# Optimization experiments

Measured on AMD Instinct MI355X. Metric: run time of the kernel, lower is better.

The kernel has to match this reference:

```python
import jax, jax.numpy as jnp
import numpy as np

LN_EPS = 1e-5

def _ln(x, g, b):
    m = jnp.mean(x, axis=-1, keepdims=True)
    v = jnp.mean(jnp.square(x - m), axis=-1, keepdims=True)
    return (x - m) / jnp.sqrt(v + LN_EPS) * g + b

def setup_inputs() -> dict:
    key = jax.random.key(0)
    ks = jax.random.split(key, 24)
    B, S, N = 8, 4096, 32
    H = 32          # self_dim // 2
    D = 64          # self_dim
    O = 32          # output_dim
    def w(k, shape):
        fan_in = shape[0]
        return jax.random.normal(k, shape, dtype=jnp.float32) / np.sqrt(fan_in)
    inp = {
        "expr": jax.random.normal(ks[0], (B, S), dtype=jnp.float32),
        "neighbors": jax.random.normal(ks[1], (B, N, S), dtype=jnp.float32),
        "edge_info": jax.random.normal(ks[2], (B, S, N), dtype=jnp.float32),
        "mask": jax.random.bernoulli(ks[3], 0.1, (B, S)),
        # neighbors branch: Linear(2,H), LN(H), ReLU, Linear(H,H)
        "nW1": w(ks[4], (2, H)), "nb1": jnp.zeros((H,), jnp.float32),
        "nlg": jnp.ones((H,), jnp.float32), "nlb": jnp.zeros((H,), jnp.float32),
        "nW2": w(ks[5], (H, H)), "nb2": jnp.zeros((H,), jnp.float32),
        # self branch: Linear(1,H), LN(H), ReLU, Linear(H,H)
        "sW1": w(ks[6], (1, H)), "sb1": jnp.zeros((H,), jnp.float32),
        "slg": jnp.ones((H,), jnp.float32), "slb": jnp.zeros((H,), jnp.float32),
        "sW2": w(ks[7], (H, H)), "sb2": jnp.zeros((H,), jnp.float32),
        # shared: Linear(D,D), LN(D), ReLU, Linear(D,O)
        "hW1": w(ks[8], (D, D)), "hb1": jnp.zeros((D,), jnp.float32),
        "hlg": jnp.ones((D,), jnp.float32), "hlb": jnp.zeros((D,), jnp.float32),
        "hW2": w(ks[9], (D, O)), "hb2": jnp.zeros((O,), jnp.float32),
    }
    return inp

def reference(expr, neighbors, edge_info, mask,
              nW1, nb1, nlg, nlb, nW2, nb2,
              sW1, sb1, slg, slb, sW2, sb2,
              hW1, hb1, hlg, hlb, hW2, hb2):
    # neighbors: (B,N,S) -> (B,S,N); pair with edge_info -> (B,S,N,2)
    nfeat = jnp.stack([jnp.transpose(neighbors, (0, 2, 1)), edge_info], axis=-1)
    h = nfeat @ nW1 + nb1                      # (B,S,N,H)
    h = jax.nn.relu(_ln(h, nlg, nlb))
    h = h @ nW2 + nb2
    nagg = jnp.sum(h, axis=-2)                 # (B,S,H)
    # self branch
    e = expr[..., None]                        # (B,S,1)
    e = e @ sW1 + sb1                          # (B,S,H)
    e = jax.nn.relu(_ln(e, slg, slb))
    e = e @ sW2 + sb2
    # shared
    x = jnp.concatenate([e, nagg], axis=-1)    # (B,S,2H)
    x = x @ hW1 + hb1
    x = jax.nn.relu(_ln(x, hlg, hlb))
    x = x @ hW2 + hb2                          # (B,S,O)
    x = jnp.where(mask[..., None], 0.0, x)
    return x
```

## Files before the change

### kernel.cpp

```cpp
#include <hip/hip_runtime.h>
#include <hip/hip_bf16.h>


#define LN_EPS 1e-5f

__global__ __launch_bounds__(256) void gnn_fold(
    const float* __restrict__ nW1, const float* __restrict__ nb1,
    const float* __restrict__ nlg, const float* __restrict__ nlb,
    const float* __restrict__ nW2, const float* __restrict__ nb2,
    const float* __restrict__ sW1, const float* __restrict__ sb1,
    const float* __restrict__ slg, const float* __restrict__ slb,
    const float* __restrict__ sW2, const float* __restrict__ sb2,
    const float* __restrict__ hW1, const float* __restrict__ hb1,
    float* __restrict__ ws)
{
    int tid = blockIdx.x * 256 + threadIdx.x;
    int k = tid >> 6, m = tid & 63;
    float acc = 0.f;
    if (k < 32) {
        #pragma unroll 8
        for (int i = 0; i < 32; ++i) acc = fmaf(sW2[k*32 + i], hW1[i*64 + m], acc);
    } else {
        int kk = k - 32;
        #pragma unroll 8
        for (int i = 0; i < 32; ++i) acc = fmaf(nW2[kk*32 + i], hW1[(32 + i)*64 + m], acc);
    }
    ws[256 + k*64 + m] = acc;

    if (blockIdx.x == 0) {
        int t = threadIdx.x;
        if (t < 64) {
            float c = hb1[t];
            for (int i = 0; i < 32; ++i) {
                c = fmaf(sb2[i], hW1[i*64 + t], c);
                c = fmaf(32.f * nb2[i], hW1[(32 + i)*64 + t], c);
            }
            ws[4352 + t] = c;
        } else if (t < 96) {
            int j = t - 64;
            float m0 = 0.f, m1 = 0.f, mb = 0.f;
            for (int i = 0; i < 32; ++i) { m0 += nW1[i]; m1 += nW1[32 + i]; mb += nb1[i]; }
            m0 *= (1.f/32.f); m1 *= (1.f/32.f); mb *= (1.f/32.f);
            float a = nW1[j] - m0, c = nW1[32 + j] - m1, d = nb1[j] - mb;
            ws[j]       = a * nlg[j];
            ws[32 + j]  = c * nlg[j];
            ws[64 + j]  = d * nlg[j];
            ws[96 + j]  = nlb[j];
            float ms = 0.f, msb = 0.f;
            for (int i = 0; i < 32; ++i) { ms += sW1[i]; msb += sb1[i]; }
            ms *= (1.f/32.f); msb *= (1.f/32.f);
            float as = sW1[j] - ms, ds = sb1[j] - msb;
            ws[136 + j] = as * slg[j];
            ws[168 + j] = ds * slg[j];
            ws[200 + j] = slb[j];
        } else if (t == 96) {
            float m0 = 0.f, m1 = 0.f, mb = 0.f;
            for (int i = 0; i < 32; ++i) { m0 += nW1[i]; m1 += nW1[32 + i]; mb += nb1[i]; }
            m0 *= (1.f/32.f); m1 *= (1.f/32.f); mb *= (1.f/32.f);
            float qaa=0,qcc=0,qdd=0,qac=0,qad=0,qcd=0;
            for (int j = 0; j < 32; ++j) {
                float a = nW1[j] - m0, c = nW1[32 + j] - m1, d = nb1[j] - mb;
                qaa += a*a; qcc += c*c; qdd += d*d; qac += a*c; qad += a*d; qcd += c*d;
            }
            ws[128]=qaa*(1.f/32.f); ws[129]=qcc*(1.f/32.f); ws[130]=qdd*(1.f/32.f);
            ws[131]=qac*(1.f/32.f); ws[132]=qad*(1.f/32.f); ws[133]=qcd*(1.f/32.f);
            float ms = 0.f, msb = 0.f;
            for (int i = 0; i < 32; ++i) { ms += sW1[i]; msb += sb1[i]; }
            ms *= (1.f/32.f); msb *= (1.f/32.f);
            float saa=0, sad=0, sdd=0;
            for (int j = 0; j < 32; ++j) {
                float as = sW1[j] - ms, ds = sb1[j] - msb;
                saa += as*as; sad += as*ds; sdd += ds*ds;
            }
            ws[232]=saa*(1.f/32.f); ws[233]=sad*(1.f/32.f); ws[234]=sdd*(1.f/32.f);
        }
    }
}

__global__ __launch_bounds__(256) void gnn_main(
    const float* __restrict__ expr, const float* __restrict__ neighbors,
    const float* __restrict__ edge_info, const int* __restrict__ mask,
    const float* __restrict__ hlg, const float* __restrict__ hlb,
    const float* __restrict__ hW2, const float* __restrict__ hb2,
    const float* __restrict__ ws, float* __restrict__ out)
{
    __shared__ float s_feat[64 * 33 * 2];
    __shared__ float s_inv[64 * 33];
    __shared__ float s_X[64 * 65];
    __shared__ float s_red[64 * 9];
    __shared__ float s_expr[64];
    __shared__ float s_prm[256];
    __shared__ float s_G[64 * 64];
    __shared__ float s_cv[64];
    __shared__ float s_h2[64 * 32];
    __shared__ float s_hb2[32];
    __shared__ float s_hlg[64];
    __shared__ float s_hlb[64];

    const int t  = threadIdx.x;
    const int g0 = blockIdx.x * 64;
    const int bb = g0 >> 12;
    const int s0 = g0 & 4095;
    const float* nbp = neighbors + ((size_t)bb * 32 * 4096 + s0);
    const float* eip = edge_info + (size_t)g0 * 32;

    if (t < 64) ((float4*)s_prm)[t] = ((const float4*)ws)[t];
    #pragma unroll
    for (int i = 0; i < 4; ++i)
        ((float4*)s_G)[i * 256 + t] = ((const float4*)(ws + 256))[i * 256 + t];
    if (t < 16) ((float4*)s_cv)[t] = ((const float4*)(ws + 4352))[t];
    #pragma unroll
    for (int i = 0; i < 2; ++i)
        ((float4*)s_h2)[i * 256 + t] = ((const float4*)hW2)[i * 256 + t];
    if (t < 32) s_hb2[t] = hb2[t];
    if (t < 64) { s_hlg[t] = hlg[t]; s_hlb[t] = hlb[t]; }

    #pragma unroll
    for (int i = 0; i < 8; ++i) {
        int idx = i * 256 + t;
        int n = idx >> 6, col = idx & 63;
        s_feat[(col * 33 + n) * 2 + 0] = nbp[n * 4096 + col];
    }
    #pragma unroll
    for (int i = 0; i < 8; ++i) {
        int idx = i * 256 + t;
        int tok = idx >> 5, n = idx & 31;
        s_feat[(tok * 33 + n) * 2 + 1] = eip[idx];
    }
    if (t < 64) s_expr[t] = expr[g0 + t];
    __syncthreads();

    {
        float qaa = s_prm[128], qcc = s_prm[129], qdd = s_prm[130];
        float qac = s_prm[131], qad = s_prm[132], qcd = s_prm[133];
        #pragma unroll
        for (int i = 0; i < 8; ++i) {
            int idx = i * 256 + t;
            int tok = idx >> 5, n = idx & 31;
            float2 f = *(const float2*)&s_feat[(tok * 33 + n) * 2];
            float nb = f.x, ei = f.y;
            float v = qdd + nb * (qaa * nb + 2.f * qad) + ei * (qcc * ei + 2.f * qcd)
                    + 2.f * qac * nb * ei;
            s_inv[tok * 33 + n] = rsqrtf(v + LN_EPS);
        }
    }
    __syncthreads();

    const int tok = t >> 2;
    const int jb  = (t & 3) * 8;
    float Ag[8], Cg[8], Dg[8], lbv[8];
    *(float4*)&Ag[0]  = *(const float4*)&s_prm[jb];
    *(float4*)&Ag[4]  = *(const float4*)&s_prm[jb + 4];
    *(float4*)&Cg[0]  = *(const float4*)&s_prm[32 + jb];
    *(float4*)&Cg[4]  = *(const float4*)&s_prm[32 + jb + 4];
    *(float4*)&Dg[0]  = *(const float4*)&s_prm[64 + jb];
    *(float4*)&Dg[4]  = *(const float4*)&s_prm[64 + jb + 4];
    *(float4*)&lbv[0] = *(const float4*)&s_prm[96 + jb];
    *(float4*)&lbv[4] = *(const float4*)&s_prm[96 + jb + 4];

    float nsum[8] = {0,0,0,0,0,0,0,0};
    #pragma unroll 4
    for (int n = 0; n < 32; ++n) {
        float2 f  = *(const float2*)&s_feat[(tok * 33 + n) * 2];
        float inv = s_inv[tok * 33 + n];
        #pragma unroll
        for (int i = 0; i < 8; ++i) {
            float r = fmaf(f.x, Ag[i], Dg[i]);
            r = fmaf(f.y, Cg[i], r);
            r = fmaf(r, inv, lbv[i]);
            nsum[i] += fmaxf(r, 0.f);
        }
    }

    {
        float As[8], Ds[8], Lb[8];
        *(float4*)&As[0] = *(const float4*)&s_prm[136 + jb];
        *(float4*)&As[4] = *(const float4*)&s_prm[136 + jb + 4];
        *(float4*)&Ds[0] = *(const float4*)&s_prm[168 + jb];
        *(float4*)&Ds[4] = *(const float4*)&s_prm[168 + jb + 4];
        *(float4*)&Lb[0] = *(const float4*)&s_prm[200 + jb];
        *(float4*)&Lb[4] = *(const float4*)&s_prm[200 + jb + 4];
        float ex  = s_expr[tok];
        float saa = s_prm[232], sad = s_prm[233], sdd = s_prm[234];
        float vs  = fmaf(ex, fmaf(ex, saa, 2.f * sad), sdd);
        float invs = rsqrtf(vs + LN_EPS);
        #pragma unroll
        for (int i = 0; i < 8; ++i) {
            float r = fmaf(ex, As[i], Ds[i]);
            r = fmaf(r, invs, Lb[i]);
            s_X[tok * 65 + jb + i]      = fmaxf(r, 0.f);
            s_X[tok * 65 + 32 + jb + i] = nsum[i];
        }
    }
    __syncthreads();

    const int w = __builtin_amdgcn_readfirstlane(t >> 6);
    const int l = t & 63;
    float y[16];
    *(float4*)&y[0]  = *(const float4*)&s_cv[w * 16];
    *(float4*)&y[4]  = *(const float4*)&s_cv[w * 16 + 4];
    *(float4*)&y[8]  = *(const float4*)&s_cv[w * 16 + 8];
    *(float4*)&y[12] = *(const float4*)&s_cv[w * 16 + 12];
    #pragma unroll 4
    for (int k = 0; k < 64; ++k) {
        float xk = s_X[l * 65 + k];
        const float* gk = &s_G[k * 64 + w * 16];
        float4 g0 = *(const float4*)&gk[0];
        float4 g1 = *(const float4*)&gk[4];
        float4 g2 = *(const float4*)&gk[8];
        float4 g3 = *(const float4*)&gk[12];
        y[0]  = fmaf(xk, g0.x, y[0]);  y[1]  = fmaf(xk, g0.y, y[1]);
        y[2]  = fmaf(xk, g0.z, y[2]);  y[3]  = fmaf(xk, g0.w, y[3]);
        y[4]  = fmaf(xk, g1.x, y[4]);  y[5]  = fmaf(xk, g1.y, y[5]);
        y[6]  = fmaf(xk, g1.z, y[6]);  y[7]  = fmaf(xk, g1.w, y[7]);
        y[8]  = fmaf(xk, g2.x, y[8]);  y[9]  = fmaf(xk, g2.y, y[9]);
        y[10] = fmaf(xk, g2.z, y[10]); y[11] = fmaf(xk, g2.w, y[11]);
        y[12] = fmaf(xk, g3.x, y[12]); y[13] = fmaf(xk, g3.y, y[13]);
        y[14] = fmaf(xk, g3.z, y[14]); y[15] = fmaf(xk, g3.w, y[15]);
    }

    float sm = 0.f, s2 = 0.f;
    #pragma unroll
    for (int i = 0; i < 16; ++i) { sm += y[i]; s2 = fmaf(y[i], y[i], s2); }
    s_red[l * 9 + w * 2 + 0] = sm;
    s_red[l * 9 + w * 2 + 1] = s2;
    __syncthreads();
    float tot = 0.f, tot2 = 0.f;
    #pragma unroll
    for (int r = 0; r < 4; ++r) {
        tot  += s_red[l * 9 + r * 2 + 0];
        tot2 += s_red[l * 9 + r * 2 + 1];
    }
    float mean = tot * (1.f / 64.f);
    float var  = tot2 * (1.f / 64.f) - mean * mean;
    float linv = rsqrtf(var + LN_EPS);
    #pragma unroll
    for (int i = 0; i < 16; ++i) {
        float v = (y[i] - mean) * linv;
        v = fmaf(v, s_hlg[w * 16 + i], s_hlb[w * 16 + i]);
        y[i] = fmaxf(v, 0.f);
    }
    #pragma unroll
    for (int i = 0; i < 16; ++i) s_X[l * 65 + w * 16 + i] = y[i];
    __syncthreads();

    const int ob = w * 8;
    float o[8];
    *(float4*)&o[0] = *(const float4*)&s_hb2[ob];
    *(float4*)&o[4] = *(const float4*)&s_hb2[ob + 4];
    #pragma unroll 4
    for (int m = 0; m < 64; ++m) {
        float ym = s_X[l * 65 + m];
        const float* h2 = &s_h2[m * 32 + ob];
        float4 h0 = *(const float4*)&h2[0];
        float4 h1 = *(const float4*)&h2[4];
        o[0] = fmaf(ym, h0.x, o[0]); o[1] = fmaf(ym, h0.y, o[1]);
        o[2] = fmaf(ym, h0.z, o[2]); o[3] = fmaf(ym, h0.w, o[3]);
        o[4] = fmaf(ym, h1.x, o[4]); o[5] = fmaf(ym, h1.y, o[5]);
        o[6] = fmaf(ym, h1.z, o[6]); o[7] = fmaf(ym, h1.w, o[7]);
    }
    int mk = mask[g0 + l];
    float4 o0 = make_float4(o[0], o[1], o[2], o[3]);
    float4 o1 = make_float4(o[4], o[5], o[6], o[7]);
    if (mk) { o0 = make_float4(0.f,0.f,0.f,0.f); o1 = o0; }
    float4* op = (float4*)(out + (size_t)(g0 + l) * 32 + ob);
    op[0] = o0;
    op[1] = o1;
}

extern "C" void kernel_launch(void* const* d_in, const int* in_sizes, int n_in,
                              void* d_out, int out_size, void* d_ws, size_t ws_size,
                              hipStream_t stream) {
    const float* expr      = (const float*)d_in[0];
    const float* neighbors = (const float*)d_in[1];
    const float* edge_info = (const float*)d_in[2];
    const int*   mask      = (const int*)d_in[3];
    const float* nW1 = (const float*)d_in[4];
    const float* nb1 = (const float*)d_in[5];
    const float* nlg = (const float*)d_in[6];
    const float* nlb = (const float*)d_in[7];
    const float* nW2 = (const float*)d_in[8];
    const float* nb2 = (const float*)d_in[9];
    const float* sW1 = (const float*)d_in[10];
    const float* sb1 = (const float*)d_in[11];
    const float* slg = (const float*)d_in[12];
    const float* slb = (const float*)d_in[13];
    const float* sW2 = (const float*)d_in[14];
    const float* sb2 = (const float*)d_in[15];
    const float* hW1 = (const float*)d_in[16];
    const float* hb1 = (const float*)d_in[17];
    const float* hlg = (const float*)d_in[18];
    const float* hlb = (const float*)d_in[19];
    const float* hW2 = (const float*)d_in[20];
    const float* hb2 = (const float*)d_in[21];
    float* ws  = (float*)d_ws;
    float* out = (float*)d_out;

    gnn_fold<<<16, 256, 0, stream>>>(nW1, nb1, nlg, nlb, nW2, nb2,
                                     sW1, sb1, slg, slb, sW2, sb2,
                                     hW1, hb1, ws);
    gnn_main<<<512, 256, 0, stream>>>(expr, neighbors, edge_info, mask,
                                      hlg, hlb, hW2, hb2, ws, out);
}
```

Baseline: 123.6 us.

## Fuse weight-folding prologue into main kernel and retile the shared-layer GEMM

Removes the separate fold kernel and has every block recompute the folded parameters (LN coefficients via wave shuffles, the 64x64 folded weight matrix, the bias vector) in shared memory, saving one launch and a global workspace round trip. The per-neighbor LN inverse-std is now computed inline in the aggregation loop, which drops a shared buffer and a barrier. The hW1 stage is retiled so each thread handles two tokens by eight outputs. The cost is redundant per-block weight folding (512 blocks each do a 64x64x32 product) plus heavier shared-memory use.

```diff
diff --git a/kernel.cpp b/kernel.cpp
--- a/kernel.cpp
+++ b/kernel.cpp
@@ -1,10 +1,11 @@
 #include <hip/hip_runtime.h>
-#include <hip/hip_bf16.h>
 
 
 #define LN_EPS 1e-5f
 
-__global__ __launch_bounds__(256) void gnn_fold(
+__global__ __launch_bounds__(256) void gnn_fused(
+    const float* __restrict__ expr, const float* __restrict__ neighbors,
+    const float* __restrict__ edge_info, const int* __restrict__ mask,
     const float* __restrict__ nW1, const float* __restrict__ nb1,
     const float* __restrict__ nlg, const float* __restrict__ nlb,
     const float* __restrict__ nW2, const float* __restrict__ nb2,
@@ -12,90 +13,17 @@
     const float* __restrict__ slg, const float* __restrict__ slb,
     const float* __restrict__ sW2, const float* __restrict__ sb2,
     const float* __restrict__ hW1, const float* __restrict__ hb1,
-    float* __restrict__ ws)
-{
-    int tid = blockIdx.x * 256 + threadIdx.x;
-    int k = tid >> 6, m = tid & 63;
-    float acc = 0.f;
-    if (k < 32) {
-        #pragma unroll 8
-        for (int i = 0; i < 32; ++i) acc = fmaf(sW2[k*32 + i], hW1[i*64 + m], acc);
-    } else {
-        int kk = k - 32;
-        #pragma unroll 8
-        for (int i = 0; i < 32; ++i) acc = fmaf(nW2[kk*32 + i], hW1[(32 + i)*64 + m], acc);
-    }
-    ws[256 + k*64 + m] = acc;
-
-    if (blockIdx.x == 0) {
-        int t = threadIdx.x;
-        if (t < 64) {
-            float c = hb1[t];
-            for (int i = 0; i < 32; ++i) {
-                c = fmaf(sb2[i], hW1[i*64 + t], c);
-                c = fmaf(32.f * nb2[i], hW1[(32 + i)*64 + t], c);
-            }
-            ws[4352 + t] = c;
-        } else if (t < 96) {
-            int j = t - 64;
-            float m0 = 0.f, m1 = 0.f, mb = 0.f;
-            for (int i = 0; i < 32; ++i) { m0 += nW1[i]; m1 += nW1[32 + i]; mb += nb1[i]; }
-            m0 *= (1.f/32.f); m1 *= (1.f/32.f); mb *= (1.f/32.f);
-            float a = nW1[j] - m0, c = nW1[32 + j] - m1, d = nb1[j] - mb;
-            ws[j]       = a * nlg[j];
-            ws[32 + j]  = c * nlg[j];
-            ws[64 + j]  = d * nlg[j];
-            ws[96 + j]  = nlb[j];
-            float ms = 0.f, msb = 0.f;
-            for (int i = 0; i < 32; ++i) { ms += sW1[i]; msb += sb1[i]; }
-            ms *= (1.f/32.f); msb *= (1.f/32.f);
-            float as = sW1[j] - ms, ds = sb1[j] - msb;
-            ws[136 + j] = as * slg[j];
-            ws[168 + j] = ds * slg[j];
-            ws[200 + j] = slb[j];
-        } else if (t == 96) {
-            float m0 = 0.f, m1 = 0.f, mb = 0.f;
-            for (int i = 0; i < 32; ++i) { m0 += nW1[i]; m1 += nW1[32 + i]; mb += nb1[i]; }
-            m0 *= (1.f/32.f); m1 *= (1.f/32.f); mb *= (1.f/32.f);
-            float qaa=0,qcc=0,qdd=0,qac=0,qad=0,qcd=0;
-            for (int j = 0; j < 32; ++j) {
-                float a = nW1[j] - m0, c = nW1[32 + j] - m1, d = nb1[j] - mb;
-                qaa += a*a; qcc += c*c; qdd += d*d; qac += a*c; qad += a*d; qcd += c*d;
-            }
-            ws[128]=qaa*(1.f/32.f); ws[129]=qcc*(1.f/32.f); ws[130]=qdd*(1.f/32.f);
-            ws[131]=qac*(1.f/32.f); ws[132]=qad*(1.f/32.f); ws[133]=qcd*(1.f/32.f);
-            float ms = 0.f, msb = 0.f;
-            for (int i = 0; i < 32; ++i) { ms += sW1[i]; msb += sb1[i]; }
-            ms *= (1.f/32.f); msb *= (1.f/32.f);
-            float saa=0, sad=0, sdd=0;
-            for (int j = 0; j < 32; ++j) {
-                float as = sW1[j] - ms, ds = sb1[j] - msb;
-                saa += as*as; sad += as*ds; sdd += ds*ds;
-            }
-            ws[232]=saa*(1.f/32.f); ws[233]=sad*(1.f/32.f); ws[234]=sdd*(1.f/32.f);
-        }
-    }
-}
-
-__global__ __launch_bounds__(256) void gnn_main(
-    const float* __restrict__ expr, const float* __restrict__ neighbors,
-    const float* __restrict__ edge_info, const int* __restrict__ mask,
     const float* __restrict__ hlg, const float* __restrict__ hlb,
     const float* __restrict__ hW2, const float* __restrict__ hb2,
-    const float* __restrict__ ws, float* __restrict__ out)
+    float* __restrict__ out)
 {
     __shared__ float s_feat[64 * 33 * 2];
-    __shared__ float s_inv[64 * 33];
     __shared__ float s_X[64 * 65];
-    __shared__ float s_red[64 * 9];
+    __shared__ float s_G[64 * 64];
+    __shared__ float s_h2[64 * 32];
+    __shared__ float s_tmp[2 * 32 * 36];
+    __shared__ float s_prm[512];
     __shared__ float s_expr[64];
-    __shared__ float s_prm[256];
-    __shared__ float s_G[64 * 64];
-    __shared__ float s_cv[64];
-    __shared__ float s_h2[64 * 32];
-    __shared__ float s_hb2[32];
-    __shared__ float s_hlg[64];
-    __shared__ float s_hlb[64];
 
     const int t  = threadIdx.x;
     const int g0 = blockIdx.x * 64;
@@ -104,17 +32,6 @@
     const float* nbp = neighbors + ((size_t)bb * 32 * 4096 + s0);
     const float* eip = edge_info + (size_t)g0 * 32;
 
-    if (t < 64) ((float4*)s_prm)[t] = ((const float4*)ws)[t];
-    #pragma unroll
-    for (int i = 0; i < 4; ++i)
-        ((float4*)s_G)[i * 256 + t] = ((const float4*)(ws + 256))[i * 256 + t];
-    if (t < 16) ((float4*)s_cv)[t] = ((const float4*)(ws + 4352))[t];
-    #pragma unroll
-    for (int i = 0; i < 2; ++i)
-        ((float4*)s_h2)[i * 256 + t] = ((const float4*)hW2)[i * 256 + t];
-    if (t < 32) s_hb2[t] = hb2[t];
-    if (t < 64) { s_hlg[t] = hlg[t]; s_hlb[t] = hlb[t]; }
-
     #pragma unroll
     for (int i = 0; i < 8; ++i) {
         int idx = i * 256 + t;
@@ -128,51 +45,134 @@
         s_feat[(tok * 33 + n) * 2 + 1] = eip[idx];
     }
     if (t < 64) s_expr[t] = expr[g0 + t];
+    #pragma unroll
+    for (int i = 0; i < 2; ++i)
+        ((float4*)s_h2)[i * 256 + t] = ((const float4*)hW2)[i * 256 + t];
+    if (t < 64) { s_prm[256 + t] = hlg[t]; s_prm[320 + t] = hlb[t]; }
+    if (t < 32) s_prm[384 + t] = hb2[t];
+    #pragma unroll
+    for (int rep = 0; rep < 4; ++rep) {
+        int idx = rep * 256 + t;
+        int i2 = idx & 31, k2 = idx >> 5;
+        s_tmp[i2 * 36 + k2]        = sW2[idx];
+        s_tmp[1152 + i2 * 36 + k2] = nW2[idx];
+    }
+
+    if (t < 32) {
+        const int j = t;
+        float w0 = nW1[j], w1 = nW1[32 + j], b1v = nb1[j];
+        float sw = sW1[j], sb = sb1[j];
+        float m0 = w0, m1 = w1, mb = b1v, ms = sw, msb = sb;
+        #pragma unroll
+        for (int off = 1; off < 32; off <<= 1) {
+            m0  += __shfl_xor(m0, off);
+            m1  += __shfl_xor(m1, off);
+            mb  += __shfl_xor(mb, off);
+            ms  += __shfl_xor(ms, off);
+            msb += __shfl_xor(msb, off);
+        }
+        m0 *= (1.f/32.f); m1 *= (1.f/32.f); mb *= (1.f/32.f);
+        ms *= (1.f/32.f); msb *= (1.f/32.f);
+        float a = w0 - m0, c = w1 - m1, d = b1v - mb;
+        float gj = nlg[j];
+        s_prm[j]      = a * gj;
+        s_prm[32 + j] = c * gj;
+        s_prm[64 + j] = d * gj;
+        s_prm[96 + j] = nlb[j];
+        float as = sw - ms, ds = sb - msb;
+        float sgj = slg[j];
+        s_prm[136 + j] = as * sgj;
+        s_prm[168 + j] = ds * sgj;
+        s_prm[200 + j] = slb[j];
+        float qaa=a*a, qcc=c*c, qdd=d*d, qac=a*c, qad=a*d, qcd=c*d;
+        float saa=as*as, sad=as*ds, sdd=ds*ds;
+        #pragma unroll
+        for (int off = 1; off < 32; off <<= 1) {
+            qaa += __shfl_xor(qaa, off); qcc += __shfl_xor(qcc, off);
+            qdd += __shfl_xor(qdd, off); qac += __shfl_xor(qac, off);
+            qad += __shfl_xor(qad, off); qcd += __shfl_xor(qcd, off);
+            saa += __shfl_xor(saa, off); sad += __shfl_xor(sad, off);
+            sdd += __shfl_xor(sdd, off);
+        }
+        if (j == 0) {
+            s_prm[128]=qaa*(1.f/32.f); s_prm[129]=qcc*(1.f/32.f); s_prm[130]=qdd*(1.f/32.f);
+            s_prm[131]=qac*(1.f/32.f); s_prm[132]=qad*(1.f/32.f); s_prm[133]=qcd*(1.f/32.f);
+            s_prm[232]=saa*(1.f/32.f); s_prm[233]=sad*(1.f/32.f); s_prm[234]=sdd*(1.f/32.f);
+        }
+    }
     __syncthreads();
 
     {
-        float qaa = s_prm[128], qcc = s_prm[129], qdd = s_prm[130];
-        float qac = s_prm[131], qad = s_prm[132], qcd = s_prm[133];
-        #pragma unroll
-        for (int i = 0; i < 8; ++i) {
-            int idx = i * 256 + t;
-            int tok = idx >> 5, n = idx & 31;
+        const int w = t >> 6;
+        const int m = t & 63;
+        const float* hcol = hW1 + m + ((w < 2) ? 0 : 32 * 64);
+        const float* wbase = (w < 2) ? (s_tmp + w * 16) : (s_tmp + 1152 + (w - 2) * 16);
+        float g[16];
+        #pragma unroll
+        for (int kk = 0; kk < 16; ++kk) g[kk] = 0.f;
+        #pragma unroll 4
+        for (int i = 0; i < 32; ++i) {
+            float hv = hcol[i * 64];
+            const float* wr = wbase + i * 36;
+            float4 wa = *(const float4*)&wr[0];
+            float4 wb = *(const float4*)&wr[4];
+            float4 wc = *(const float4*)&wr[8];
+            float4 wd = *(const float4*)&wr[12];
+            g[0]=fmaf(wa.x,hv,g[0]);  g[1]=fmaf(wa.y,hv,g[1]);
+            g[2]=fmaf(wa.z,hv,g[2]);  g[3]=fmaf(wa.w,hv,g[3]);
+            g[4]=fmaf(wb.x,hv,g[4]);  g[5]=fmaf(wb.y,hv,g[5]);
+            g[6]=fmaf(wb.z,hv,g[6]);  g[7]=fmaf(wb.w,hv,g[7]);
+            g[8]=fmaf(wc.x,hv,g[8]);  g[9]=fmaf(wc.y,hv,g[9]);
+            g[10]=fmaf(wc.z,hv,g[10]); g[11]=fmaf(wc.w,hv,g[11]);
+            g[12]=fmaf(wd.x,hv,g[12]); g[13]=fmaf(wd.y,hv,g[13]);
+            g[14]=fmaf(wd.z,hv,g[14]); g[15]=fmaf(wd.w,hv,g[15]);
+        }
+        const int k0 = w * 16;
+        #pragma unroll
+        for (int kk = 0; kk < 16; ++kk) s_G[(k0 + kk) * 64 + m] = g[kk];
+    }
+    if (t >= 192) {
+        const int m = t - 192;
+        float c = hb1[m];
+        #pragma unroll 4
+        for (int i = 0; i < 32; ++i) {
+            c = fmaf(sb2[i], hW1[i * 64 + m], c);
+            c = fmaf(32.f * nb2[i], hW1[(32 + i) * 64 + m], c);
+        }
+        s_prm[416 + m] = c;
+    }
+
+    {
+        const int tok = t >> 2;
+        const int jb  = (t & 3) * 8;
+        float Ag[8], Cg[8], Dg[8], lbv[8];
+        *(float4*)&Ag[0]  = *(const float4*)&s_prm[jb];
+        *(float4*)&Ag[4]  = *(const float4*)&s_prm[jb + 4];
+        *(float4*)&Cg[0]  = *(const float4*)&s_prm[32 + jb];
+        *(float4*)&Cg[4]  = *(const float4*)&s_prm[32 + jb + 4];
+        *(float4*)&Dg[0]  = *(const float4*)&s_prm[64 + jb];
+        *(float4*)&Dg[4]  = *(const float4*)&s_prm[64 + jb + 4];
+        *(float4*)&lbv[0] = *(const float4*)&s_prm[96 + jb];
+        *(float4*)&lbv[4] = *(const float4*)&s_prm[96 + jb + 4];
+        const float qaa = s_prm[128], qcc = s_prm[129], qdd = s_prm[130];
+        const float qac = s_prm[131], qad = s_prm[132], qcd = s_prm[133];
+
+        float nsum[8] = {0,0,0,0,0,0,0,0};
+        #pragma unroll 4
+        for (int n = 0; n < 32; ++n) {
             float2 f = *(const float2*)&s_feat[(tok * 33 + n) * 2];
-            float nb = f.x, ei = f.y;
-            float v = qdd + nb * (qaa * nb + 2.f * qad) + ei * (qcc * ei + 2.f * qcd)
-                    + 2.f * qac * nb * ei;
-            s_inv[tok * 33 + n] = rsqrtf(v + LN_EPS);
-        }
-    }
-    __syncthreads();
-
-    const int tok = t >> 2;
-    const int jb  = (t & 3) * 8;
-    float Ag[8], Cg[8], Dg[8], lbv[8];
-    *(float4*)&Ag[0]  = *(const float4*)&s_prm[jb];
-    *(float4*)&Ag[4]  = *(const float4*)&s_prm[jb + 4];
-    *(float4*)&Cg[0]  = *(const float4*)&s_prm[32 + jb];
-    *(float4*)&Cg[4]  = *(const float4*)&s_prm[32 + jb + 4];
-    *(float4*)&Dg[0]  = *(const float4*)&s_prm[64 + jb];
-    *(float4*)&Dg[4]  = *(const float4*)&s_prm[64 + jb + 4];
-    *(float4*)&lbv[0] = *(const float4*)&s_prm[96 + jb];
-    *(float4*)&lbv[4] = *(const float4*)&s_prm[96 + jb + 4];
-
-    float nsum[8] = {0,0,0,0,0,0,0,0};
-    #pragma unroll 4
-    for (int n = 0; n < 32; ++n) {
-        float2 f  = *(const float2*)&s_feat[(tok * 33 + n) * 2];
-        float inv = s_inv[tok * 33 + n];
-        #pragma unroll
-        for (int i = 0; i < 8; ++i) {
-            float r = fmaf(f.x, Ag[i], Dg[i]);
-            r = fmaf(f.y, Cg[i], r);
-            r = fmaf(r, inv, lbv[i]);
-            nsum[i] += fmaxf(r, 0.f);
-        }
-    }
-
-    {
+            float v = qdd + f.x * fmaf(qaa, f.x, 2.f * qad)
+                    + f.y * fmaf(qcc, f.y, 2.f * qcd)
+                    + 2.f * qac * f.x * f.y;
+            float inv = rsqrtf(v + LN_EPS);
+            #pragma unroll
+            for (int i = 0; i < 8; ++i) {
+                float r = fmaf(f.x, Ag[i], Dg[i]);
+                r = fmaf(f.y, Cg[i], r);
+                r = fmaf(r, inv, lbv[i]);
+                nsum[i] += fmaxf(r, 0.f);
+            }
+        }
         float As[8], Ds[8], Lb[8];
         *(float4*)&As[0] = *(const float4*)&s_prm[136 + jb];
         *(float4*)&As[4] = *(const float4*)&s_prm[136 + jb + 4];
@@ -180,9 +180,8 @@
         *(float4*)&Ds[4] = *(const float4*)&s_prm[168 + jb + 4];
         *(float4*)&Lb[0] = *(const float4*)&s_prm[200 + jb];
         *(float4*)&Lb[4] = *(const float4*)&s_prm[200 + jb + 4];
-        float ex  = s_expr[tok];
-        float saa = s_prm[232], sad = s_prm[233], sdd = s_prm[234];
-        float vs  = fmaf(ex, fmaf(ex, saa, 2.f * sad), sdd);
+        float ex = s_expr[tok];
+        float vs = fmaf(ex, fmaf(ex, s_prm[232], 2.f * s_prm[233]), s_prm[234]);
         float invs = rsqrtf(vs + LN_EPS);
         #pragma unroll
         for (int i = 0; i < 8; ++i) {
@@ -194,83 +193,113 @@
     }
     __syncthreads();
 
-    const int w = __builtin_amdgcn_readfirstlane(t >> 6);
-    const int l = t & 63;
-    float y[16];
-    *(float4*)&y[0]  = *(const float4*)&s_cv[w * 16];
-    *(float4*)&y[4]  = *(const float4*)&s_cv[w * 16 + 4];
-    *(float4*)&y[8]  = *(const float4*)&s_cv[w * 16 + 8];
-    *(float4*)&y[12] = *(const float4*)&s_cv[w * 16 + 12];
+    const int w4 = __builtin_amdgcn_readfirstlane(t >> 6);
+    const int l  = t & 63;
+    const int gi = w4 * 2 + (l >> 5);
+    const int tl = (l & 31) * 2;
+    float y0[8], y1[8];
+    {
+        float4 c0 = *(const float4*)&s_prm[416 + 8 * gi];
+        float4 c1 = *(const float4*)&s_prm[416 + 8 * gi + 4];
+        y0[0]=c0.x; y0[1]=c0.y; y0[2]=c0.z; y0[3]=c0.w;
+        y0[4]=c1.x; y0[5]=c1.y; y0[6]=c1.z; y0[7]=c1.w;
+        #pragma unroll
+        for (int i = 0; i < 8; ++i) y1[i] = y0[i];
+    }
     #pragma unroll 4
     for (int k = 0; k < 64; ++k) {
-        float xk = s_X[l * 65 + k];
-        const float* gk = &s_G[k * 64 + w * 16];
-        float4 g0 = *(const float4*)&gk[0];
-        float4 g1 = *(const float4*)&gk[4];
-        float4 g2 = *(const float4*)&gk[8];
-        float4 g3 = *(const float4*)&gk[12];
-        y[0]  = fmaf(xk, g0.x, y[0]);  y[1]  = fmaf(xk, g0.y, y[1]);
-        y[2]  = fmaf(xk, g0.z, y[2]);  y[3]  = fmaf(xk, g0.w, y[3]);
-        y[4]  = fmaf(xk, g1.x, y[4]);  y[5]  = fmaf(xk, g1.y, y[5]);
-        y[6]  = fmaf(xk, g1.z, y[6]);  y[7]  = fmaf(xk, g1.w, y[7]);
-        y[8]  = fmaf(xk, g2.x, y[8]);  y[9]  = fmaf(xk, g2.y, y[9]);
-        y[10] = fmaf(xk, g2.z, y[10]); y[11] = fmaf(xk, g2.w, y[11]);
-        y[12] = fmaf(xk, g3.x, y[12]); y[13] = fmaf(xk, g3.y, y[13]);
-        y[14] = fmaf(xk, g3.z, y[14]); y[15] = fmaf(xk, g3.w, y[15]);
-    }
-
-    float sm = 0.f, s2 = 0.f;
-    #pragma unroll
-    for (int i = 0; i < 16; ++i) { sm += y[i]; s2 = fmaf(y[i], y[i], s2); }
-    s_red[l * 9 + w * 2 + 0] = sm;
-    s_red[l * 9 + w * 2 + 1] = s2;
+        float xa = s_X[tl * 65 + k];
+        float xb = s_X[(tl + 1) * 65 + k];
+        const float* gk = &s_G[k * 64 + 8 * gi];
+        float4 ga = *(const float4*)&gk[0];
+        float4 gb = *(const float4*)&gk[4];
+        y0[0]=fmaf(xa,ga.x,y0[0]); y0[1]=fmaf(xa,ga.y,y0[1]);
+        y0[2]=fmaf(xa,ga.z,y0[2]); y0[3]=fmaf(xa,ga.w,y0[3]);
+        y0[4]=fmaf(xa,gb.x,y0[4]); y0[5]=fmaf(xa,gb.y,y0[5]);
+        y0[6]=fmaf(xa,gb.z,y0[6]); y0[7]=fmaf(xa,gb.w,y0[7]);
+        y1[0]=fmaf(xb,ga.x,y1[0]); y1[1]=fmaf(xb,ga.y,y1[1]);
+        y1[2]=fmaf(xb,ga.z,y1[2]); y1[3]=fmaf(xb,ga.w,y1[3]);
+        y1[4]=fmaf(xb,gb.x,y1[4]); y1[5]=fmaf(xb,gb.y,y1[5]);
+        y1[6]=fmaf(xb,gb.z,y1[6]); y1[7]=fmaf(xb,gb.w,y1[7]);
+    }
+    {
+        float sm0=0, ss0=0, sm1=0, ss1=0;
+        #pragma unroll
+        for (int i = 0; i < 8; ++i) {
+            sm0 += y0[i]; ss0 = fmaf(y0[i], y0[i], ss0);
+            sm1 += y1[i]; ss1 = fmaf(y1[i], y1[i], ss1);
+        }
+        s_tmp[tl * 20 + gi * 2 + 0]       = sm0;
+        s_tmp[tl * 20 + gi * 2 + 1]       = ss0;
+        s_tmp[(tl + 1) * 20 + gi * 2 + 0] = sm1;
+        s_tmp[(tl + 1) * 20 + gi * 2 + 1] = ss1;
+    }
     __syncthreads();
-    float tot = 0.f, tot2 = 0.f;
-    #pragma unroll
-    for (int r = 0; r < 4; ++r) {
-        tot  += s_red[l * 9 + r * 2 + 0];
-        tot2 += s_red[l * 9 + r * 2 + 1];
-    }
-    float mean = tot * (1.f / 64.f);
-    float var  = tot2 * (1.f / 64.f) - mean * mean;
-    float linv = rsqrtf(var + LN_EPS);
-    #pragma unroll
-    for (int i = 0; i < 16; ++i) {
-        float v = (y[i] - mean) * linv;
-        v = fmaf(v, s_hlg[w * 16 + i], s_hlb[w * 16 + i]);
-        y[i] = fmaxf(v, 0.f);
-    }
-    #pragma unroll
-    for (int i = 0; i < 16; ++i) s_X[l * 65 + w * 16 + i] = y[i];
+    {
+        float4 p0 = *(const float4*)&s_tmp[tl * 20 + 0];
+        float4 p1 = *(const float4*)&s_tmp[tl * 20 + 4];
+        float4 p2 = *(const float4*)&s_tmp[tl * 20 + 8];
+        float4 p3 = *(const float4*)&s_tmp[tl * 20 + 12];
+        float tot0  = p0.x + p0.z + p1.x + p1.z + p2.x + p2.z + p3.x + p3.z;
+        float tsq0  = p0.y + p0.w + p1.y + p1.w + p2.y + p2.w + p3.y + p3.w;
+        float4 q0 = *(const float4*)&s_tmp[(tl + 1) * 20 + 0];
+        float4 q1 = *(const float4*)&s_tmp[(tl + 1) * 20 + 4];
+        float4 q2 = *(const float4*)&s_tmp[(tl + 1) * 20 + 8];
+        float4 q3 = *(const float4*)&s_tmp[(tl + 1) * 20 + 12];
+        float tot1  = q0.x + q0.z + q1.x + q1.z + q2.x + q2.z + q3.x + q3.z;
+        float tsq1  = q0.y + q0.w + q1.y + q1.w + q2.y + q2.w + q3.y + q3.w;
+        float mean0 = tot0 * (1.f/64.f);
+        float var0  = tsq0 * (1.f/64.f) - mean0 * mean0;
+        float li0   = rsqrtf(var0 + LN_EPS);
+        float mean1 = tot1 * (1.f/64.f);
+        float var1  = tsq1 * (1.f/64.f) - mean1 * mean1;
+        float li1   = rsqrtf(var1 + LN_EPS);
+        float4 lg0 = *(const float4*)&s_prm[256 + 8 * gi];
+        float4 lg1 = *(const float4*)&s_prm[256 + 8 * gi + 4];
+        float4 lb0 = *(const float4*)&s_prm[320 + 8 * gi];
+        float4 lb1 = *(const float4*)&s_prm[320 + 8 * gi + 4];
+        float lg[8] = {lg0.x,lg0.y,lg0.z,lg0.w,lg1.x,lg1.y,lg1.z,lg1.w};
+        float lb[8] = {lb0.x,lb0.y,lb0.z,lb0.w,lb1.x,lb1.y,lb1.z,lb1.w};
+        #pragma unroll
+        for (int i = 0; i < 8; ++i) {
+            float v0 = fmaf((y0[i] - mean0) * li0, lg[i], lb[i]);
+            float v1 = fmaf((y1[i] - mean1) * li1, lg[i], lb[i]);
+            s_X[tl * 65 + 8 * gi + i]       = fmaxf(v0, 0.f);
+            s_X[(tl + 1) * 65 + 8 * gi + i] = fmaxf(v1, 0.f);
+        }
+    }
     __syncthreads();
 
-    const int ob = w * 8;
-    float o[8];
-    *(float4*)&o[0] = *(const float4*)&s_hb2[ob];
-    *(float4*)&o[4] = *(const float4*)&s_hb2[ob + 4];
-    #pragma unroll 4
-    for (int m = 0; m < 64; ++m) {
-        float ym = s_X[l * 65 + m];
-        const float* h2 = &s_h2[m * 32 + ob];
-        float4 h0 = *(const float4*)&h2[0];
-        float4 h1 = *(const float4*)&h2[4];
-        o[0] = fmaf(ym, h0.x, o[0]); o[1] = fmaf(ym, h0.y, o[1]);
-        o[2] = fmaf(ym, h0.z, o[2]); o[3] = fmaf(ym, h0.w, o[3]);
-        o[4] = fmaf(ym, h1.x, o[4]); o[5] = fmaf(ym, h1.y, o[5]);
-        o[6] = fmaf(ym, h1.z, o[6]); o[7] = fmaf(ym, h1.w, o[7]);
-    }
-    int mk = mask[g0 + l];
-    float4 o0 = make_float4(o[0], o[1], o[2], o[3]);
-    float4 o1 = make_float4(o[4], o[5], o[6], o[7]);
-    if (mk) { o0 = make_float4(0.f,0.f,0.f,0.f); o1 = o0; }
-    float4* op = (float4*)(out + (size_t)(g0 + l) * 32 + ob);
-    op[0] = o0;
-    op[1] = o1;
+    {
+        const int ob = w4 * 8;
+        float o[8];
+        *(float4*)&o[0] = *(const float4*)&s_prm[384 + ob];
+        *(float4*)&o[4] = *(const float4*)&s_prm[384 + ob + 4];
+        #pragma unroll 4
+        for (int m = 0; m < 64; ++m) {
+            float ym = s_X[l * 65 + m];
+            const float* h2 = &s_h2[m * 32 + ob];
+            float4 h0 = *(const float4*)&h2[0];
+            float4 h1 = *(const float4*)&h2[4];
+            o[0]=fmaf(ym,h0.x,o[0]); o[1]=fmaf(ym,h0.y,o[1]);
+            o[2]=fmaf(ym,h0.z,o[2]); o[3]=fmaf(ym,h0.w,o[3]);
+            o[4]=fmaf(ym,h1.x,o[4]); o[5]=fmaf(ym,h1.y,o[5]);
+            o[6]=fmaf(ym,h1.z,o[6]); o[7]=fmaf(ym,h1.w,o[7]);
+        }
+        int mk = mask[g0 + l];
+        float4 o0 = make_float4(o[0], o[1], o[2], o[3]);
+        float4 o1 = make_float4(o[4], o[5], o[6], o[7]);
+        if (mk) { o0 = make_float4(0.f,0.f,0.f,0.f); o1 = o0; }
+        float4* op = (float4*)(out + (size_t)(g0 + l) * 32 + ob);
+        op[0] = o0;
+        op[1] = o1;
+    }
 }
 
 extern "C" void kernel_launch(void* const* d_in, const int* in_sizes, int n_in,
                               void* d_out, int out_size, void* d_ws, size_t ws_size,
                               hipStream_t stream) {
+    (void)in_sizes; (void)n_in; (void)out_size; (void)d_ws; (void)ws_size;
     const float* expr      = (const float*)d_in[0];
     const float* neighbors = (const float*)d_in[1];
     const float* edge_info = (const float*)d_in[2];
@@ -293,12 +322,10 @@
     const float* hlb = (const float*)d_in[19];
     const float* hW2 = (const float*)d_in[20];
     const float* hb2 = (const float*)d_in[21];
-    float* ws  = (float*)d_ws;
-    float* out = (float*)d_out;
-
-    gnn_fold<<<16, 256, 0, stream>>>(nW1, nb1, nlg, nlb, nW2, nb2,
-                                     sW1, sb1, slg, slb, sW2, sb2,
-                                     hW1, hb1, ws);
-    gnn_main<<<512, 256, 0, stream>>>(expr, neighbors, edge_info, mask,
-                                      hlg, hlb, hW2, hb2, ws, out);
+    float* outp = (float*)d_out;
+
+    gnn_fused<<<512, 256, 0, stream>>>(expr, neighbors, edge_info, mask,
+                                       nW1, nb1, nlg, nlb, nW2, nb2,
+                                       sW1, sb1, slg, slb, sW2, sb2,
+                                       hW1, hb1, hlg, hlb, hW2, hb2, outp);
 }
```

Result: no change. 122.3 us (-1.0%).
